# Optimization experiments

Measured on AMD Instinct MI355X. Metric: run time of the kernel, lower is better.

## Reference

```python
import jax, jax.numpy as jnp
import numpy as np

L, D, H, FF, T, B = 8, 1024, 16, 4096, 2048, 2
HD = D // H
EPS_NORM = 1e-5
EPS_LN = 1e-5


def setup_inputs() -> dict:
    key = jax.random.key(0)
    ks = jax.random.split(key, 8)
    s = 0.02
    return {
        "q": jax.random.normal(ks[0], (B, T, D), jnp.float32),
        "pos_emb": jax.random.uniform(ks[1], (T, D), jnp.float32, -0.05, 0.05),
        "Wqkv": jax.random.normal(ks[2], (L, 3 * D, D), jnp.float32) * s,
        "conv_w": 1.0 + jax.random.normal(ks[3], (L, 3 * D), jnp.float32) * s,
        "proj_w": jax.random.normal(ks[4], (L, D, D), jnp.float32) * s,
        "fc_w": jax.random.normal(ks[5], (L, FF, D), jnp.float32) * s,
        "mlp_w": jax.random.normal(ks[6], (L, D, FF), jnp.float32) * s,
        "gamma": jnp.ones((D,), jnp.float32),
    }


def _l2norm(x):
    # torch F.normalize: x / clamp_min(||x||_2, eps)
    n = jnp.sqrt(jnp.sum(x * x, axis=-1, keepdims=True))
    return x / jnp.maximum(n, EPS_NORM)


def _block(x, Wqkv_i, conv_i, proj_i, fc_i, mlp_i):
    Bb, Tt, _ = x.shape
    # W_qkv linear followed by depthwise 1x1 conv == per-channel scale
    qkv = jnp.einsum("btd,ed->bte", x, Wqkv_i) * conv_i  # [B,T,3D]
    qh, kh, vh = jnp.split(qkv, 3, axis=-1)
    qh = qh.reshape(Bb, Tt, H, HD).transpose(0, 2, 1, 3)  # [B,H,T,hd]
    kh = kh.reshape(Bb, Tt, H, HD).transpose(0, 2, 1, 3)
    vh = vh.reshape(Bb, Tt, H, HD).transpose(0, 2, 1, 3)
    qh = _l2norm(qh)
    kh = _l2norm(kh)
    scores = jnp.einsum("bhqd,bhkd->bhqk", qh, kh) / jnp.sqrt(jnp.float32(HD))
    causal = jnp.tril(jnp.ones((Tt, Tt), bool))
    scores = jnp.where(causal, scores, jnp.finfo(scores.dtype).min)
    attn = jax.nn.softmax(scores, axis=-1)
    y = jnp.einsum("bhqk,bhkd->bhqd", attn, vh)
    y = y.transpose(0, 2, 1, 3).reshape(Bb, Tt, D)
    y = jnp.einsum("btd,ed->bte", y, proj_i)
    x = x + y
    h = jax.nn.gelu(jnp.einsum("btd,fd->btf", x, fc_i), approximate=False)
    h = jnp.einsum("btf,df->btd", h, mlp_i)
    return x + h


def reference(q, pos_emb, Wqkv, conv_w, proj_w, fc_w, mlp_w, gamma):
    x = q + pos_emb[: q.shape[-2], :]
    for i in range(L):
        x = _block(x, Wqkv[i], conv_w[i], proj_w[i], fc_w[i], mlp_w[i])
    mu = jnp.mean(x, axis=-1, keepdims=True)
    var = jnp.mean(jnp.square(x - mu), axis=-1, keepdims=True)
    return (x - mu) / jnp.sqrt(var + EPS_LN) * gamma
```

## Files before the change

### kernel.cpp

```cpp
#include <hip/hip_runtime.h>
#include <math.h>

typedef unsigned short u16;
typedef unsigned int u32;
typedef __attribute__((ext_vector_type(8))) short s16x8;
typedef __attribute__((ext_vector_type(4))) float f32x4;
typedef __attribute__((ext_vector_type(4))) u16 u16x4;

#define B_ 2
#define T_ 2048
#define D_ 1024
#define H_ 16
#define HD_ 64
#define FF_ 4096
#define L_ 8

__device__ __forceinline__ u16 f2b(float f) {
  u32 u = __builtin_bit_cast(u32, f);
  u += 0x7fffu + ((u >> 16) & 1u);
  return (u16)(u >> 16);
}
__device__ __forceinline__ float b2f(u16 h) {
  u32 u = ((u32)h) << 16;
  return __builtin_bit_cast(float, u);
}

__device__ __forceinline__ void load_lds16(const u16* g, u16* l) {
  __builtin_amdgcn_global_load_lds(
      (const __attribute__((address_space(1))) u32*)g,
      (__attribute__((address_space(3))) u32*)l, 16, 0, 0);
}

__global__ __launch_bounds__(256) void fold_qkv_kernel(
    const float* __restrict__ W, const float* __restrict__ conv, u16* __restrict__ out) {
  size_t idx = ((size_t)blockIdx.x * 256 + threadIdx.x) * 4;
  size_t row = idx >> 10;
  float scale = conv[row];
  f32x4 v = *(const f32x4*)&W[idx];
  u16x4 h;
  h.x = f2b(v.x * scale); h.y = f2b(v.y * scale);
  h.z = f2b(v.z * scale); h.w = f2b(v.w * scale);
  *(u16x4*)&out[idx] = h;
}

__global__ __launch_bounds__(256) void cast_kernel(
    const float* __restrict__ in, u16* __restrict__ out) {
  size_t idx = ((size_t)blockIdx.x * 256 + threadIdx.x) * 4;
  f32x4 v = *(const f32x4*)&in[idx];
  u16x4 h;
  h.x = f2b(v.x); h.y = f2b(v.y); h.z = f2b(v.z); h.w = f2b(v.w);
  *(u16x4*)&out[idx] = h;
}

__global__ __launch_bounds__(256) void posadd_kernel(
    const float* __restrict__ q, const float* __restrict__ pos,
    float* __restrict__ xf, u16* __restrict__ xb) {
  size_t idx = ((size_t)blockIdx.x * 256 + threadIdx.x) * 4;
  size_t td = idx & ((size_t)T_ * D_ - 1);
  f32x4 a = *(const f32x4*)&q[idx];
  f32x4 p = *(const f32x4*)&pos[td];
  f32x4 v = a + p;
  *(f32x4*)&xf[idx] = v;
  u16x4 h;
  h.x = f2b(v.x); h.y = f2b(v.y); h.z = f2b(v.z); h.w = f2b(v.w);
  *(u16x4*)&xb[idx] = h;
}

template <int EPI>
__global__ __launch_bounds__(256, 2) void gemm_bt(
    const u16* __restrict__ A, const u16* __restrict__ Bt,
    float* __restrict__ Cf, u16* __restrict__ Cb,
    const float* __restrict__ resid, int M, int N, int K) {
  __shared__ u16 As[128 * 32];
  __shared__ u16 Bs[128 * 32];
  const int tid = threadIdx.x;
  const int lane = tid & 63;
  const int w = tid >> 6;
  const int wr = w >> 1, wc = w & 1;
  const size_t row0 = (size_t)blockIdx.y * 128;
  const size_t col0 = (size_t)blockIdx.x * 128;

  const u16* Ag = A + row0 * K;
  const u16* Bg = Bt + col0 * K;

  f32x4 zero = {0.f, 0.f, 0.f, 0.f};
  f32x4 acc[4][4];
#pragma unroll
  for (int m = 0; m < 4; ++m)
#pragma unroll
    for (int n = 0; n < 4; ++n) acc[m][n] = zero;

  const int chunk0 = w * 2, chunk1 = w * 2 + 1;
  const int e0 = chunk0 * 512 + lane * 8;
  const int e1 = chunk1 * 512 + lane * 8;
  const int r0 = e0 >> 5, c0 = e0 & 31;
  const int r1 = e1 >> 5, c1 = e1 & 31;

  const int fr = lane & 15;
  const int koff = (lane >> 4) * 8;

  for (int k0 = 0; k0 < K; k0 += 32) {
    __syncthreads();
    load_lds16(Ag + (size_t)r0 * K + k0 + c0, &As[chunk0 * 512]);
    load_lds16(Ag + (size_t)r1 * K + k0 + c1, &As[chunk1 * 512]);
    load_lds16(Bg + (size_t)r0 * K + k0 + c0, &Bs[chunk0 * 512]);
    load_lds16(Bg + (size_t)r1 * K + k0 + c1, &Bs[chunk1 * 512]);
    __syncthreads();

    s16x8 a[4], b[4];
#pragma unroll
    for (int m = 0; m < 4; ++m)
      a[m] = *(const s16x8*)&As[(wr * 64 + m * 16 + fr) * 32 + koff];
#pragma unroll
    for (int n = 0; n < 4; ++n)
      b[n] = *(const s16x8*)&Bs[(wc * 64 + n * 16 + fr) * 32 + koff];
#pragma unroll
    for (int m = 0; m < 4; ++m)
#pragma unroll
      for (int n = 0; n < 4; ++n)
        acc[m][n] = __builtin_amdgcn_mfma_f32_16x16x32_bf16(a[m], b[n], acc[m][n], 0, 0, 0);
  }

  const int rq = (lane >> 4) * 4;
#pragma unroll
  for (int m = 0; m < 4; ++m) {
#pragma unroll
    for (int n = 0; n < 4; ++n) {
      size_t col = col0 + wc * 64 + n * 16 + fr;
#pragma unroll
      for (int r = 0; r < 4; ++r) {
        size_t row = row0 + wr * 64 + m * 16 + rq + r;
        size_t idx = row * (size_t)N + col;
        float v = acc[m][n][r];
        if (EPI == 0) {
          Cf[idx] = v;
        } else if (EPI == 1) {
          float o = resid[idx] + v;
          Cf[idx] = o;
          Cb[idx] = f2b(o);
        } else if (EPI == 2) {
          float g = 0.5f * v * (1.0f + erff(v * 0.70710678118654752f));
          Cb[idx] = f2b(g);
        } else {
          Cb[idx] = f2b(v);
        }
      }
    }
  }
}

__global__ __launch_bounds__(256) void qkvnorm_kernel(
    const u16* __restrict__ qkv, u16* __restrict__ qb, u16* __restrict__ kb,
    u16* __restrict__ vb) {
  int gid = blockIdx.x * 4 + (threadIdx.x >> 6);
  int lane = threadIdx.x & 63;
  int h = gid & (H_ - 1);
  int t = (gid >> 4) & (T_ - 1);
  int b = gid >> 15;
  const u16* base = qkv + ((size_t)(b * T_ + t)) * (3 * D_) + h * HD_;
  float qv = b2f(base[lane]);
  float kv = b2f(base[D_ + lane]);
  u16 vv = base[2 * D_ + lane];
  float qs = qv * qv, ks = kv * kv;
#pragma unroll
  for (int off = 1; off < 64; off <<= 1) {
    qs += __shfl_xor(qs, off);
    ks += __shfl_xor(ks, off);
  }
  float qn = qv / fmaxf(sqrtf(qs), 1e-5f);
  float kn = kv / fmaxf(sqrtf(ks), 1e-5f);
  size_t oi = ((size_t)(b * H_ + h) * T_ + t) * HD_ + lane;
  qb[oi] = f2b(qn);
  kb[oi] = f2b(kn);
  vb[oi] = vv;
}

__global__ __launch_bounds__(256, 2) void attn_kernel(
    const u16* __restrict__ qg, const u16* __restrict__ kg,
    const u16* __restrict__ vg, u16* __restrict__ y) {
  __shared__ u16 Ks[64 * 72];
  __shared__ u16 Vt[64 * 72];
  __shared__ u16 Ps[4][16 * 72];

  const int tid = threadIdx.x;
  const int lane = tid & 63;
  const int w = tid >> 6;
  const int qt = blockIdx.x;
  const int bh = blockIdx.y;
  const int b = bh >> 4, hh = bh & 15;

  const u16* Q = qg + ((size_t)bh * T_ + qt * 64) * HD_;
  const u16* Kb = kg + (size_t)bh * T_ * HD_;
  const u16* Vb = vg + (size_t)bh * T_ * HD_;

  const int fr = lane & 15;
  const int koff = (lane >> 4) * 8;

  s16x8 qf0 = *(const s16x8*)&Q[(w * 16 + fr) * 64 + koff];
  s16x8 qf1 = *(const s16x8*)&Q[(w * 16 + fr) * 64 + 32 + koff];

  f32x4 zero = {0.f, 0.f, 0.f, 0.f};
  f32x4 o[4];
#pragma unroll
  for (int n = 0; n < 4; ++n) o[n] = zero;
  float mrow[4] = {-1e30f, -1e30f, -1e30f, -1e30f};
  float lrow[4] = {0.f, 0.f, 0.f, 0.f};

  for (int kt = 0; kt <= qt; ++kt) {
    __syncthreads();
    {
      const u16* Kg = Kb + (size_t)kt * 64 * 64;
      const u16* Vg = Vb + (size_t)kt * 64 * 64;
#pragma unroll
      for (int it = 0; it < 2; ++it) {
        int e = (tid * 2 + it) * 8;
        int r = e >> 6, c = e & 63;
        s16x8 kv = *(const s16x8*)&Kg[e];
        *(s16x8*)&Ks[r * 72 + c] = kv;
        s16x8 vv = *(const s16x8*)&Vg[e];
#pragma unroll
        for (int j = 0; j < 8; ++j) Vt[(c + j) * 72 + r] = (u16)vv[j];
      }
    }
    __syncthreads();

    f32x4 s[4];
#pragma unroll
    for (int n = 0; n < 4; ++n) {
      s16x8 kf0 = *(const s16x8*)&Ks[(n * 16 + fr) * 72 + koff];
      s16x8 kf1 = *(const s16x8*)&Ks[(n * 16 + fr) * 72 + 32 + koff];
      f32x4 z = zero;
      z = __builtin_amdgcn_mfma_f32_16x16x32_bf16(qf0, kf0, z, 0, 0, 0);
      z = __builtin_amdgcn_mfma_f32_16x16x32_bf16(qf1, kf1, z, 0, 0, 0);
      s[n] = z;
    }

    const int grow_base = qt * 64 + w * 16 + (lane >> 4) * 4;
    const int gcol_base = kt * 64 + fr;
    float p[4][4];
#pragma unroll
    for (int r = 0; r < 4; ++r) {
      float mx = -1e30f;
#pragma unroll
      for (int n = 0; n < 4; ++n) {
        float sv = s[n][r] * 0.125f;
        if (gcol_base + n * 16 > grow_base + r) sv = -1e30f;
        s[n][r] = sv;
        mx = fmaxf(mx, sv);
      }
#pragma unroll
      for (int off = 1; off < 16; off <<= 1) mx = fmaxf(mx, __shfl_xor(mx, off));
      float mnew = fmaxf(mrow[r], mx);
      float sc = __expf(mrow[r] - mnew);
      float rs = 0.f;
#pragma unroll
      for (int n = 0; n < 4; ++n) {
        float pv = __expf(s[n][r] - mnew);
        p[n][r] = pv;
        rs += pv;
      }
#pragma unroll
      for (int off = 1; off < 16; off <<= 1) rs += __shfl_xor(rs, off);
      lrow[r] = lrow[r] * sc + rs;
      mrow[r] = mnew;
#pragma unroll
      for (int n = 0; n < 4; ++n) o[n][r] *= sc;
    }

    u16* Pw = &Ps[w][0];
#pragma unroll
    for (int n = 0; n < 4; ++n)
#pragma unroll
      for (int r = 0; r < 4; ++r)
        Pw[((lane >> 4) * 4 + r) * 72 + n * 16 + fr] = f2b(p[n][r]);
    asm volatile("s_waitcnt lgkmcnt(0)" ::: "memory");

    s16x8 pa0 = *(const s16x8*)&Pw[fr * 72 + koff];
    s16x8 pa1 = *(const s16x8*)&Pw[fr * 72 + 32 + koff];
#pragma unroll
    for (int n = 0; n < 4; ++n) {
      s16x8 v0 = *(const s16x8*)&Vt[(n * 16 + fr) * 72 + koff];
      s16x8 v1 = *(const s16x8*)&Vt[(n * 16 + fr) * 72 + 32 + koff];
      o[n] = __builtin_amdgcn_mfma_f32_16x16x32_bf16(pa0, v0, o[n], 0, 0, 0);
      o[n] = __builtin_amdgcn_mfma_f32_16x16x32_bf16(pa1, v1, o[n], 0, 0, 0);
    }
  }

#pragma unroll
  for (int n = 0; n < 4; ++n)
#pragma unroll
    for (int r = 0; r < 4; ++r) {
      int grow = qt * 64 + w * 16 + (lane >> 4) * 4 + r;
      float val = o[n][r] / lrow[r];
      y[((size_t)b * T_ + grow) * D_ + hh * 64 + n * 16 + fr] = f2b(val);
    }
}

__global__ __launch_bounds__(256) void ln_kernel(
    const float* __restrict__ x, const float* __restrict__ gamma,
    float* __restrict__ out) {
  int row = blockIdx.x;
  int tid = threadIdx.x;
  const float* xr = x + (size_t)row * D_;
  f32x4 v = *(const f32x4*)&xr[tid * 4];
  float s = v.x + v.y + v.z + v.w;
  float ss = v.x * v.x + v.y * v.y + v.z * v.z + v.w * v.w;
#pragma unroll
  for (int off = 1; off < 64; off <<= 1) {
    s += __shfl_xor(s, off);
    ss += __shfl_xor(ss, off);
  }
  __shared__ float red[8];
  int w = tid >> 6, lane = tid & 63;
  if (lane == 0) {
    red[w] = s;
    red[4 + w] = ss;
  }
  __syncthreads();
  s = red[0] + red[1] + red[2] + red[3];
  ss = red[4] + red[5] + red[6] + red[7];
  float mu = s * (1.f / D_);
  float var = ss * (1.f / D_) - mu * mu;
  float rstd = rsqrtf(var + 1e-5f);
  f32x4 g = *(const f32x4*)&gamma[tid * 4];
  f32x4 o;
  o.x = (v.x - mu) * rstd * g.x;
  o.y = (v.y - mu) * rstd * g.y;
  o.z = (v.z - mu) * rstd * g.z;
  o.w = (v.w - mu) * rstd * g.w;
  *(f32x4*)&out[(size_t)row * D_ + tid * 4] = o;
}

extern "C" void kernel_launch(void* const* d_in, const int* in_sizes, int n_in,
                              void* d_out, int out_size, void* d_ws, size_t ws_size,
                              hipStream_t stream) {
  (void)in_sizes; (void)n_in; (void)out_size; (void)ws_size;
  const float* q = (const float*)d_in[0];
  const float* pos = (const float*)d_in[1];
  const float* Wqkv = (const float*)d_in[2];
  const float* convw = (const float*)d_in[3];
  const float* projw = (const float*)d_in[4];
  const float* fcw = (const float*)d_in[5];
  const float* mlpw = (const float*)d_in[6];
  const float* gamma = (const float*)d_in[7];
  float* out = (float*)d_out;

  char* ws = (char*)d_ws;
  size_t off = 0;
  auto alloc = [&](size_t bytes) {
    char* p = ws + off;
    off += (bytes + 255) & ~(size_t)255;
    return p;
  };
  const size_t nWq = (size_t)3 * D_ * D_;
  const size_t nPr = (size_t)D_ * D_;
  const size_t nFc = (size_t)FF_ * D_;
  const size_t nMl = (size_t)D_ * FF_;
  const size_t nX = (size_t)B_ * T_ * D_;
  const size_t nQKV = (size_t)B_ * T_ * 3 * D_;
  const size_t nH = (size_t)B_ * T_ * FF_;

  u16* Wqb = (u16*)alloc(nWq * 2);
  u16* Prb = (u16*)alloc(nPr * 2);
  u16* Fcb = (u16*)alloc(nFc * 2);
  u16* Mlb = (u16*)alloc(nMl * 2);
  float* xf = (float*)alloc(nX * 4);
  u16* xb = (u16*)alloc(nX * 2);
  size_t shared_bytes = nH * 2 > nQKV * 2 ? nH * 2 : nQKV * 2;
  u16* qkvb = (u16*)alloc(shared_bytes);
  u16* hb = qkvb;
  u16* qb = (u16*)alloc(nX * 2);
  u16* kb = (u16*)alloc(nX * 2);
  u16* vb = (u16*)alloc(nX * 2);
  u16* yb = (u16*)alloc(nX * 2);

  posadd_kernel<<<nX / 1024, 256, 0, stream>>>(q, pos, xf, xb);

  const int M = B_ * T_;
  for (int l = 0; l < L_; ++l) {
    fold_qkv_kernel<<<nWq / 1024, 256, 0, stream>>>(
        Wqkv + (size_t)l * nWq, convw + (size_t)l * 3 * D_, Wqb);
    cast_kernel<<<nPr / 1024, 256, 0, stream>>>(projw + (size_t)l * nPr, Prb);
    cast_kernel<<<nFc / 1024, 256, 0, stream>>>(fcw + (size_t)l * nFc, Fcb);
    cast_kernel<<<nMl / 1024, 256, 0, stream>>>(mlpw + (size_t)l * nMl, Mlb);

    gemm_bt<3><<<dim3(3 * D_ / 128, M / 128), 256, 0, stream>>>(
        xb, Wqb, nullptr, qkvb, nullptr, M, 3 * D_, D_);
    qkvnorm_kernel<<<(B_ * T_ * H_) / 4, 256, 0, stream>>>(qkvb, qb, kb, vb);
    attn_kernel<<<dim3(T_ / 64, B_ * H_), 256, 0, stream>>>(qb, kb, vb, yb);
    gemm_bt<1><<<dim3(D_ / 128, M / 128), 256, 0, stream>>>(
        yb, Prb, xf, xb, xf, M, D_, D_);
    gemm_bt<2><<<dim3(FF_ / 128, M / 128), 256, 0, stream>>>(
        xb, Fcb, nullptr, hb, nullptr, M, FF_, D_);
    gemm_bt<1><<<dim3(D_ / 128, M / 128), 256, 0, stream>>>(
        hb, Mlb, xf, xb, xf, M, D_, FF_);
  }
  ln_kernel<<<B_ * T_, 256, 0, stream>>>(xf, gamma, out);
}
```

Before: 3.167 ms.

## Pre-transpose V in a separate kernel and use 128-row query tiles in attention

A new kernel writes V in [bh, d, t] layout so the attention loop stages V into shared memory with plain vector copies instead of scalar scatter transposes. The attention block grows to 512 threads covering 128 query rows, so each staged K/V tile serves twice as many queries. The cost is an extra launch, an extra buffer, and extra global traffic for the transpose. Blocks now do twice the work, giving fewer and longer blocks and coarser causal load balance.

```diff
diff --git a/kernel.cpp b/kernel.cpp
--- a/kernel.cpp
+++ b/kernel.cpp
@@ -175,12 +175,38 @@
   vb[oi] = vv;
 }
 
-__global__ __launch_bounds__(256, 2) void attn_kernel(
+__global__ __launch_bounds__(256) void vtrans_kernel(
+    const u16* __restrict__ vb, u16* __restrict__ vt) {
+  __shared__ u16 tile[64 * 72];
+  const int bh = blockIdx.y;
+  const int t0 = blockIdx.x * 64;
+  const int tid = threadIdx.x;
+  const u16* src = vb + ((size_t)bh * T_ + t0) * HD_;
+#pragma unroll
+  for (int it = 0; it < 2; ++it) {
+    int e = (tid * 2 + it) * 8;
+    int r = e >> 6, c = e & 63;
+    s16x8 v = *(const s16x8*)&src[(size_t)r * HD_ + c];
+    *(s16x8*)&tile[r * 72 + c] = v;
+  }
+  __syncthreads();
+#pragma unroll
+  for (int it = 0; it < 2; ++it) {
+    int e = (tid * 2 + it) * 8;
+    int d = e >> 6, c = e & 63;
+    u16 tmp[8];
+#pragma unroll
+    for (int j = 0; j < 8; ++j) tmp[j] = tile[(c + j) * 72 + d];
+    *(s16x8*)&vt[((size_t)bh * HD_ + d) * T_ + t0 + c] = *(const s16x8*)tmp;
+  }
+}
+
+__global__ __launch_bounds__(512) void attn_kernel(
     const u16* __restrict__ qg, const u16* __restrict__ kg,
-    const u16* __restrict__ vg, u16* __restrict__ y) {
+    const u16* __restrict__ vtg, u16* __restrict__ y) {
   __shared__ u16 Ks[64 * 72];
   __shared__ u16 Vt[64 * 72];
-  __shared__ u16 Ps[4][16 * 72];
+  __shared__ u16 Ps[8][16 * 72];
 
   const int tid = threadIdx.x;
   const int lane = tid & 63;
@@ -189,15 +215,15 @@
   const int bh = blockIdx.y;
   const int b = bh >> 4, hh = bh & 15;
 
-  const u16* Q = qg + ((size_t)bh * T_ + qt * 64) * HD_;
+  const u16* Q = qg + ((size_t)bh * T_ + qt * 128) * HD_;
   const u16* Kb = kg + (size_t)bh * T_ * HD_;
-  const u16* Vb = vg + (size_t)bh * T_ * HD_;
+  const u16* Vg = vtg + (size_t)bh * HD_ * T_;
 
   const int fr = lane & 15;
   const int koff = (lane >> 4) * 8;
 
-  s16x8 qf0 = *(const s16x8*)&Q[(w * 16 + fr) * 64 + koff];
-  s16x8 qf1 = *(const s16x8*)&Q[(w * 16 + fr) * 64 + 32 + koff];
+  s16x8 qf0 = *(const s16x8*)&Q[(w * 16 + fr) * HD_ + koff];
+  s16x8 qf1 = *(const s16x8*)&Q[(w * 16 + fr) * HD_ + 32 + koff];
 
   f32x4 zero = {0.f, 0.f, 0.f, 0.f};
   f32x4 o[4];
@@ -206,21 +232,17 @@
   float mrow[4] = {-1e30f, -1e30f, -1e30f, -1e30f};
   float lrow[4] = {0.f, 0.f, 0.f, 0.f};
 
-  for (int kt = 0; kt <= qt; ++kt) {
+  const int sr = tid >> 3;
+  const int sc = (tid & 7) * 8;
+
+  const int ktmax = 2 * qt + 1;
+  for (int kt = 0; kt <= ktmax; ++kt) {
     __syncthreads();
     {
-      const u16* Kg = Kb + (size_t)kt * 64 * 64;
-      const u16* Vg = Vb + (size_t)kt * 64 * 64;
-#pragma unroll
-      for (int it = 0; it < 2; ++it) {
-        int e = (tid * 2 + it) * 8;
-        int r = e >> 6, c = e & 63;
-        s16x8 kv = *(const s16x8*)&Kg[e];
-        *(s16x8*)&Ks[r * 72 + c] = kv;
-        s16x8 vv = *(const s16x8*)&Vg[e];
-#pragma unroll
-        for (int j = 0; j < 8; ++j) Vt[(c + j) * 72 + r] = (u16)vv[j];
-      }
+      s16x8 kv = *(const s16x8*)&Kb[((size_t)kt * 64 + sr) * HD_ + sc];
+      *(s16x8*)&Ks[sr * 72 + sc] = kv;
+      s16x8 vv = *(const s16x8*)&Vg[(size_t)sr * T_ + kt * 64 + sc];
+      *(s16x8*)&Vt[sr * 72 + sc] = vv;
     }
     __syncthreads();
 
@@ -235,7 +257,7 @@
       s[n] = z;
     }
 
-    const int grow_base = qt * 64 + w * 16 + (lane >> 4) * 4;
+    const int grow_base = qt * 128 + w * 16 + (lane >> 4) * 4;
     const int gcol_base = kt * 64 + fr;
     float p[4][4];
 #pragma unroll
@@ -251,7 +273,7 @@
 #pragma unroll
       for (int off = 1; off < 16; off <<= 1) mx = fmaxf(mx, __shfl_xor(mx, off));
       float mnew = fmaxf(mrow[r], mx);
-      float sc = __expf(mrow[r] - mnew);
+      float sc2 = __expf(mrow[r] - mnew);
       float rs = 0.f;
 #pragma unroll
       for (int n = 0; n < 4; ++n) {
@@ -261,10 +283,10 @@
       }
 #pragma unroll
       for (int off = 1; off < 16; off <<= 1) rs += __shfl_xor(rs, off);
-      lrow[r] = lrow[r] * sc + rs;
+      lrow[r] = lrow[r] * sc2 + rs;
       mrow[r] = mnew;
 #pragma unroll
-      for (int n = 0; n < 4; ++n) o[n][r] *= sc;
+      for (int n = 0; n < 4; ++n) o[n][r] *= sc2;
     }
 
     u16* Pw = &Ps[w][0];
@@ -290,7 +312,7 @@
   for (int n = 0; n < 4; ++n)
 #pragma unroll
     for (int r = 0; r < 4; ++r) {
-      int grow = qt * 64 + w * 16 + (lane >> 4) * 4 + r;
+      int grow = qt * 128 + w * 16 + (lane >> 4) * 4 + r;
       float val = o[n][r] / lrow[r];
       y[((size_t)b * T_ + grow) * D_ + hh * 64 + n * 16 + fr] = f2b(val);
     }
@@ -372,6 +394,7 @@
   u16* qb = (u16*)alloc(nX * 2);
   u16* kb = (u16*)alloc(nX * 2);
   u16* vb = (u16*)alloc(nX * 2);
+  u16* vtb = (u16*)alloc(nX * 2);
   u16* yb = (u16*)alloc(nX * 2);
 
   posadd_kernel<<<nX / 1024, 256, 0, stream>>>(q, pos, xf, xb);
@@ -387,7 +410,8 @@
     gemm_bt<3><<<dim3(3 * D_ / 128, M / 128), 256, 0, stream>>>(
         xb, Wqb, nullptr, qkvb, nullptr, M, 3 * D_, D_);
     qkvnorm_kernel<<<(B_ * T_ * H_) / 4, 256, 0, stream>>>(qkvb, qb, kb, vb);
-    attn_kernel<<<dim3(T_ / 64, B_ * H_), 256, 0, stream>>>(qb, kb, vb, yb);
+    vtrans_kernel<<<dim3(T_ / 64, B_ * H_), 256, 0, stream>>>(vb, vtb);
+    attn_kernel<<<dim3(T_ / 128, B_ * H_), 512, 0, stream>>>(qb, kb, vtb, yb);
     gemm_bt<1><<<dim3(D_ / 128, M / 128), 256, 0, stream>>>(
         yb, Prb, xf, xb, xf, M, D_, D_);
     gemm_bt<2><<<dim3(FF_ / 128, M / 128), 256, 0, stream>>>(
```

After: 3.006 ms. -5.1%, faster.
